# Performance work log

Hardware: AMD Instinct MI355X
Metric: run time of the kernel (lower is better)

Reference implementation:

```python
import jax, jax.numpy as jnp
import numpy as np

B, S, D = 32, 512, 512      # batch, seq_len, d_model
H, K = 16, 32               # head_num, head_dim
A = 256                     # attention_hidden_dim


def setup_inputs() -> dict:
    key = jax.random.key(0)
    ks = jax.random.split(key, 10)
    s = lambda fan_in: 1.0 / np.sqrt(fan_in)
    return {
        "x":   jax.random.normal(ks[0], (B, S, D), dtype=jnp.float32),
        # per-head Q projections: Linear(D, D), stored [H, in, out]
        "Qw":  jax.random.normal(ks[1], (H, D, D), dtype=jnp.float32) * s(D),
        "Qb":  jax.random.normal(ks[2], (H, D), dtype=jnp.float32) * s(D),
        # per-head V projections: Linear(D, K)
        "Vw":  jax.random.normal(ks[3], (H, D, K), dtype=jnp.float32) * s(D),
        "Vb":  jax.random.normal(ks[4], (H, K), dtype=jnp.float32) * s(D),
        # additive attention pooling: Linear(H*K, A) then Linear(A, 1)
        "Wv":  jax.random.normal(ks[5], (H * K, A), dtype=jnp.float32) * s(H * K),
        "bv":  jax.random.normal(ks[6], (A,), dtype=jnp.float32) * s(H * K),
        "wq":  jax.random.normal(ks[7], (A, 1), dtype=jnp.float32) * s(A),
        "bq":  jax.random.normal(ks[8], (1,), dtype=jnp.float32) * s(A),
    }


def reference(x, Qw, Qb, Vw, Vb, Wv, bv, wq, bq):
    # per-head query projection: [B, H, S, D]
    q = jnp.einsum("bsd,hde->bhse", x, Qw) + Qb[None, :, None, :]
    # raw scores: [B, H, S, S] (s = query pos, t = key pos)
    scores = jnp.einsum("bhse,bte->bhst", q, x)
    # NOTE: softmax over dim=-2 (the QUERY axis), not the usual key axis
    attn = jax.nn.softmax(scores, axis=-2)
    # context: [B, H, S, D]
    ctx = jnp.einsum("bhst,btd->bhsd", attn, x)
    # per-head value projection then concat heads -> [B, S, H*K]
    head_out = jnp.einsum("bhsd,hdk->bshk", ctx, Vw) + Vb[None, None, :, :]
    h = head_out.reshape(B, S, H * K)
    # dropout is identity at inference
    # additive attention pooling
    a = jnp.tanh(h @ Wv + bv) @ wq + bq          # [B, S, 1]
    z = jnp.einsum("bs,bsk->bk", a[..., 0], h)   # [B, H*K]
    return z
```

## Files before the change

kernel.cpp:

```cpp
#include <hip/hip_runtime.h>

#define DEVFN __device__ __forceinline__

typedef _Float16 f16;
typedef _Float16 f16x8 __attribute__((ext_vector_type(8)));
typedef _Float16 f16x4 __attribute__((ext_vector_type(4)));
typedef _Float16 f16x2 __attribute__((ext_vector_type(2)));
typedef float    f32x4 __attribute__((ext_vector_type(4)));

enum { NB = 32, NS = 512, ND = 512, NH = 16, NK = 32, NA = 256 };

#define SZ(x) ((size_t)(x))

typedef __attribute__((address_space(3))) void       as3_void;
typedef const __attribute__((address_space(1))) void as1_cvoid;
DEVFN void ldsdma16(const void* g, void* l) {
  __builtin_amdgcn_global_load_lds((as1_cvoid*)g, (as3_void*)l, 16, 0, 0);
}

DEVFN int xcd_swz(int flat, int n) {
  return (flat & 7) * (n >> 3) + (flat >> 3);
}

DEVFN void gemm256_pipe(const f16* __restrict__ Ag, const f16* __restrict__ Bg,
                        int lda, int ldb, f16* smem, f32x4 acc[8][4]) {
  const int tid  = threadIdx.x;
  const int lane = tid & 63;
  const int wid  = tid >> 6;
  const int wr   = wid >> 2;
  const int wcn  = wid & 3;
  const int s_r    = tid >> 2;
  const int s_gsrc = (tid & 3) ^ (s_r & 3);
  const int frow = lane & 15;
  const int fg   = lane >> 4;

  auto stage = [&](int t) {
    f16* buf = smem + (t & 3) * 16384;
    const f16* As = Ag + t * 32;
    const f16* Bs = Bg + t * 32;
#pragma unroll
    for (int j = 0; j < 2; ++j)
      ldsdma16(As + SZ(j * 128 + s_r) * lda + s_gsrc * 8, buf + j * 4096 + tid * 8);
#pragma unroll
    for (int j = 0; j < 2; ++j)
      ldsdma16(Bs + SZ(j * 128 + s_r) * ldb + s_gsrc * 8, buf + 8192 + j * 4096 + tid * 8);
  };

  stage(0); stage(1); stage(2);

  for (int t = 0; t < 16; ++t) {
    if (t <= 13)      asm volatile("s_waitcnt vmcnt(8)" ::: "memory");
    else if (t == 14) asm volatile("s_waitcnt vmcnt(4)" ::: "memory");
    else              asm volatile("s_waitcnt vmcnt(0)" ::: "memory");
    __builtin_amdgcn_s_barrier();
    if (t < 13) stage(t + 3);

    const f16* bufA = smem + (t & 3) * 16384;
    const f16* bufB = bufA + 8192;
    f16x8 af[8], bf[4];
#pragma unroll
    for (int mi = 0; mi < 8; ++mi) {
      int r_ = wr * 128 + mi * 16 + frow;
      af[mi] = *(const f16x8*)(bufA + r_ * 32 + ((fg ^ (r_ & 3)) * 8));
    }
#pragma unroll
    for (int ni = 0; ni < 4; ++ni) {
      int r_ = wcn * 64 + ni * 16 + frow;
      bf[ni] = *(const f16x8*)(bufB + r_ * 32 + ((fg ^ (r_ & 3)) * 8));
    }
    __builtin_amdgcn_s_setprio(1);
#pragma unroll
    for (int mi = 0; mi < 8; ++mi)
#pragma unroll
      for (int ni = 0; ni < 4; ++ni)
        acc[mi][ni] = __builtin_amdgcn_mfma_f32_16x16x32_f16(af[mi], bf[ni], acc[mi][ni], 0, 0, 0);
    __builtin_amdgcn_s_setprio(0);
  }
}

DEVFN void gemm_core_128(const f16* __restrict__ Ag, const f16* __restrict__ Bg,
                         int lda, int ldb, int nk, f16* lds, f32x4 acc[4][4]) {
  f16* As = lds;
  f16* Bs = lds + 128 * 64;
  const int tid  = threadIdx.x;
  const int lane = tid & 63;
  const int wvid = tid >> 6, wr = wvid >> 1, wc = wvid & 1;
  const int srow = tid >> 3, scol = (tid & 7) * 8;
  const int frow = lane & 15, fk = (lane >> 4) * 8;
  for (int ks = 0; ks < nk; ++ks) {
    const f16* ga = Ag + ks * 64 + scol;
    const f16* gb = Bg + ks * 64 + scol;
#pragma unroll
    for (int r = 0; r < 4; ++r) {
      ldsdma16(ga + SZ(r * 32 + srow) * lda, As + SZ(r * 32 + srow) * 64 + scol);
      ldsdma16(gb + SZ(r * 32 + srow) * ldb, Bs + SZ(r * 32 + srow) * 64 + scol);
    }
    __syncthreads();
#pragma unroll
    for (int kk = 0; kk < 64; kk += 32) {
      f16x8 a[4], b[4];
#pragma unroll
      for (int i = 0; i < 4; ++i)
        a[i] = *(const f16x8*)(As + SZ(wr * 64 + i * 16 + frow) * 64 + kk + fk);
#pragma unroll
      for (int j = 0; j < 4; ++j)
        b[j] = *(const f16x8*)(Bs + SZ(wc * 64 + j * 16 + frow) * 64 + kk + fk);
#pragma unroll
      for (int i = 0; i < 4; ++i)
#pragma unroll
        for (int j = 0; j < 4; ++j)
          acc[i][j] = __builtin_amdgcn_mfma_f32_16x16x32_f16(a[i], b[j], acc[i][j], 0, 0, 0);
    }
    __syncthreads();
  }
}

DEVFN void wlds_write(f16* wlds, int row, int col, f16 v) {
  int byte = (row * 256 + col * 2) ^ ((row & 7) << 4);
  *(f16*)((char*)wlds + byte) = v;
}
DEVFN f16x8 wlds_read8(const f16* wlds, int row, int col) {
  int byte = (row * 256 + col * 2) ^ ((row & 7) << 4);
  return *(const f16x8*)((const char*)wlds + byte);
}

__global__ __launch_bounds__(256) void k_cast4(const float* __restrict__ s,
                                               f16* __restrict__ d, int n4) {
  int i = blockIdx.x * 256 + threadIdx.x;
  if (i >= n4) return;
  float4 v = ((const float4*)s)[i];
  f16x4 o; o[0] = (f16)v.x; o[1] = (f16)v.y; o[2] = (f16)v.z; o[3] = (f16)v.w;
  ((f16x4*)d)[i] = o;
}

__global__ void k_tcast(const float* __restrict__ src, f16* __restrict__ dst,
                        int R, int C, long sStride, long dStride) {
  __shared__ float tile[32][33];
  src += (long)blockIdx.z * sStride;
  dst += (long)blockIdx.z * dStride;
  int c0 = blockIdx.x * 32, r0 = blockIdx.y * 32;
  int tx = threadIdx.x, ty = threadIdx.y;
#pragma unroll
  for (int i = 0; i < 4; ++i)
    tile[ty + 8 * i][tx] = src[(long)(r0 + ty + 8 * i) * C + c0 + tx];
  __syncthreads();
#pragma unroll
  for (int i = 0; i < 4; ++i)
    dst[(long)(c0 + ty + 8 * i) * R + r0 + tx] = (f16)tile[tx][ty + 8 * i];
}

__global__ __launch_bounds__(256) void k_gemm_xv(const f16* __restrict__ xh,
                                                 const f16* __restrict__ vwt,
                                                 f16* __restrict__ xvt) {
  __shared__ f16 smem[128 * 64 * 2];
  int z = blockIdx.z, b = z >> 2, hg = z & 3, tm = blockIdx.x;
  f32x4 acc[4][4] = {};
  gemm_core_128(xh + SZ(b) * NS * ND + SZ(tm) * 128 * ND,
                vwt + SZ(hg) * 4 * NK * ND, ND, ND, ND / 64, smem, acc);
  int tid = threadIdx.x, lane = tid & 63, wvid = tid >> 6, wr = wvid >> 1, wc = wvid & 1;
  int rbase = (lane >> 4) * 4, cbase = lane & 15;
#pragma unroll
  for (int mi = 0; mi < 4; ++mi)
#pragma unroll
    for (int ni = 0; ni < 4; ++ni) {
      int n = wc * 64 + ni * 16 + cbase;
      int hh = hg * 4 + (n >> 5), kk = n & 31;
#pragma unroll
      for (int r = 0; r < 4; ++r) {
        int t = tm * 128 + wr * 64 + mi * 16 + rbase + r;
        xvt[(SZ(b * NH + hh) * NK + kk) * NS + t] = (f16)acc[mi][ni][r];
      }
    }
}

__global__ __launch_bounds__(512, 2) void k_gemm_q256(const f16* __restrict__ xh,
                                                      const f16* __restrict__ qwt,
                                                      const float* __restrict__ Qb,
                                                      f16* __restrict__ qc, int b0) {
  __shared__ f16 smem[65536];
  int n = gridDim.x;
  int lg = xcd_swz(blockIdx.x, n);
  int tm2 = lg & 1, tn2 = (lg >> 1) & 1, bhl = lg >> 2;
  int b = b0 + (bhl >> 4), h = bhl & 15;
  f32x4 acc[8][4] = {};
  gemm256_pipe(xh + SZ(b) * NS * ND + SZ(tm2) * 256 * ND,
               qwt + SZ(h) * ND * ND + SZ(tn2) * 256 * ND, ND, ND, smem, acc);
  int lane = threadIdx.x & 63, wid = threadIdx.x >> 6;
  int wr = wid >> 2, wcn = wid & 3;
  int rbase = (lane >> 4) * 4, cbase = lane & 15;
  f16* qb = qc + SZ(bhl) * NS * ND;
#pragma unroll
  for (int mi = 0; mi < 8; ++mi)
#pragma unroll
    for (int ni = 0; ni < 4; ++ni) {
      int colg = tn2 * 256 + wcn * 64 + ni * 16 + cbase;
      float bias = Qb[h * ND + colg];
#pragma unroll
      for (int r = 0; r < 4; ++r) {
        int rowg = tm2 * 256 + wr * 128 + mi * 16 + rbase + r;
        qb[SZ(rowg) * ND + colg] = (f16)(acc[mi][ni][r] + bias);
      }
    }
}

__global__ __launch_bounds__(512, 2) void k_scores256(const f16* __restrict__ qc,
                                                      const f16* __restrict__ xh,
                                                      f16* __restrict__ sc,
                                                      float* __restrict__ mp,
                                                      float* __restrict__ zp, int b0) {
  __shared__ f16 smem[65536];
  int n = gridDim.x;
  int lg = xcd_swz(blockIdx.x, n);
  int st2 = lg & 1, tt2 = (lg >> 1) & 1, bhl = lg >> 2;
  int b = b0 + (bhl >> 4);
  f32x4 acc[8][4] = {};
  gemm256_pipe(qc + SZ(bhl) * NS * ND + SZ(st2) * 256 * ND,
               xh + SZ(b) * NS * ND + SZ(tt2) * 256 * ND, ND, ND, smem, acc);
  int tid = threadIdx.x, lane = tid & 63, wid = tid >> 6;
  int wr = wid >> 2, wcn = wid & 3;
  __syncthreads();
  float* sbuf = (float*)smem;

  float mh[4];
#pragma unroll
  for (int ni = 0; ni < 4; ++ni) {
    float m = -1e30f;
#pragma unroll
    for (int mi = 0; mi < 8; ++mi)
#pragma unroll
      for (int r = 0; r < 4; ++r) m = fmaxf(m, acc[mi][ni][r]);
    m = fmaxf(m, __shfl_xor(m, 16));
    m = fmaxf(m, __shfl_xor(m, 32));
    mh[ni] = m;
  }
  if (lane < 16) {
#pragma unroll
    for (int ni = 0; ni < 4; ++ni)
      sbuf[wr * 256 + wcn * 64 + ni * 16 + lane] = mh[ni];
  }
  __syncthreads();
  int cb_ = lane & 15;
  float tmc[4];
#pragma unroll
  for (int ni = 0; ni < 4; ++ni) {
    int col = wcn * 64 + ni * 16 + cb_;
    tmc[ni] = fmaxf(sbuf[col], sbuf[256 + col]);
  }
  f16x4* scb = (f16x4*)(sc + SZ(lg) * 65536);
  float sm[4] = {0.f, 0.f, 0.f, 0.f};
#pragma unroll
  for (int mi = 0; mi < 8; ++mi)
#pragma unroll
    for (int ni = 0; ni < 4; ++ni) {
      f16x4 o;
#pragma unroll
      for (int r = 0; r < 4; ++r) {
        float ev = __expf(acc[mi][ni][r] - tmc[ni]);
        o[r] = (f16)ev;
        sm[ni] += ev;
      }
      scb[((wid * 8 + mi) * 4 + ni) * 64 + lane] = o;
    }
#pragma unroll
  for (int ni = 0; ni < 4; ++ni) {
    sm[ni] += __shfl_xor(sm[ni], 16);
    sm[ni] += __shfl_xor(sm[ni], 32);
  }
  if (lane < 16) {
#pragma unroll
    for (int ni = 0; ni < 4; ++ni)
      sbuf[512 + wr * 256 + wcn * 64 + ni * 16 + lane] = sm[ni];
  }
  __syncthreads();
  if (tid < 256) {
    float m  = fmaxf(sbuf[tid], sbuf[256 + tid]);
    float zz = sbuf[512 + tid] + sbuf[768 + tid];
    size_t idx = (SZ(bhl) * 2 + st2) * NS + tt2 * 256 + tid;
    mp[idx] = m; zp[idx] = zz;
  }
}

__global__ __launch_bounds__(256) void k_stats_combine(const float* __restrict__ mp,
                                                       const float* __restrict__ zp,
                                                       float* __restrict__ cs) {
  int i = blockIdx.x * 256 + threadIdx.x;
  int bhl = i >> 9, t = i & (NS - 1);
  float m0 = mp[(SZ(bhl) * 2 + 0) * NS + t];
  float m1 = mp[(SZ(bhl) * 2 + 1) * NS + t];
  float m = fmaxf(m0, m1);
  float e0 = __expf(m0 - m), e1 = __expf(m1 - m);
  float Z = zp[(SZ(bhl) * 2 + 0) * NS + t] * e0 + zp[(SZ(bhl) * 2 + 1) * NS + t] * e1;
  float rZ = 1.0f / Z;
  cs[(SZ(bhl) * 2 + 0) * NS + t] = e0 * rZ;
  cs[(SZ(bhl) * 2 + 1) * NS + t] = e1 * rZ;
}

__global__ __launch_bounds__(256) void k_norm_pv(const f16* __restrict__ sc,
                                                 const f16* __restrict__ xvt,
                                                 const float* __restrict__ cs,
                                                 const float* __restrict__ Vb,
                                                 f16* __restrict__ h16, int b0) {
  __shared__ f16 wlds[128 * 128];
  int bhl = blockIdx.y, b = b0 + (bhl >> 4), h = bhl & 15;
  int st = blockIdx.x;
  int tid = threadIdx.x, lane = tid & 63, wvid = tid >> 6, wr = wvid >> 1, wc = wvid & 1;
  int rbase = (lane >> 4) * 4, cbase = lane & 15, fk = (lane >> 4) * 8;
  f32x4 acc2[2][2] = {};
  const f16* xvh = xvt + SZ(b * NH + h) * NK * NS;
  for (int tt = 0; tt < 4; ++tt) {
    int blk = (bhl * 2 + (tt >> 1)) * 2 + (st >> 1);
    const f16x4* scb = (const f16x4*)(sc + SZ(blk) * 65536);
    int wave_sc = (st & 1) * 4 + ((tt & 1) * 2 + wc);
#pragma unroll
    for (int ni = 0; ni < 4; ++ni) {
      int tl = wc * 64 + ni * 16 + cbase;
      float csv = cs[(SZ(bhl) * 2 + (st >> 1)) * NS + tt * 128 + tl];
#pragma unroll
      for (int mi = 0; mi < 4; ++mi) {
        int mi_sc = wr * 4 + mi;
        f16x4 v = scb[((wave_sc * 8 + mi_sc) * 4 + ni) * 64 + lane];
#pragma unroll
        for (int r = 0; r < 4; ++r) {
          int sl = wr * 64 + mi * 16 + rbase + r;
          wlds_write(wlds, sl, tl, (f16)((float)v[r] * csv));
        }
      }
    }
    __syncthreads();
    const f16* xvb = xvh + tt * 128;
#pragma unroll
    for (int tc = 0; tc < 4; ++tc) {
      f16x8 aw[2], bx[2];
#pragma unroll
      for (int m2 = 0; m2 < 2; ++m2)
        aw[m2] = wlds_read8(wlds, wvid * 32 + m2 * 16 + cbase, tc * 32 + fk);
#pragma unroll
      for (int n2 = 0; n2 < 2; ++n2)
        bx[n2] = *(const f16x8*)(xvb + SZ(n2 * 16 + cbase) * NS + tc * 32 + fk);
#pragma unroll
      for (int m2 = 0; m2 < 2; ++m2)
#pragma unroll
        for (int n2 = 0; n2 < 2; ++n2)
          acc2[m2][n2] = __builtin_amdgcn_mfma_f32_16x16x32_f16(aw[m2], bx[n2], acc2[m2][n2], 0, 0, 0);
    }
    __syncthreads();
  }
  const float* vb = Vb + h * NK;
#pragma unroll
  for (int m2 = 0; m2 < 2; ++m2)
#pragma unroll
    for (int n2 = 0; n2 < 2; ++n2)
#pragma unroll
      for (int r = 0; r < 4; ++r) {
        int sg = st * 128 + wvid * 32 + m2 * 16 + rbase + r;
        int kk = n2 * 16 + cbase;
        float val = acc2[m2][n2][r] + vb[kk];
        h16[SZ(b * NS + sg) * (NH * NK) + h * NK + kk] = (f16)val;
      }
}

__global__ __launch_bounds__(256) void k_gemm_u(const f16* __restrict__ h16,
                                                const f16* __restrict__ wvt,
                                                const float* __restrict__ bv,
                                                f16* __restrict__ U) {
  __shared__ f16 smem[128 * 64 * 2];
  int tm = blockIdx.x, tn = blockIdx.y;
  f32x4 acc[4][4] = {};
  gemm_core_128(h16 + SZ(tm) * 128 * ND, wvt + SZ(tn) * 128 * ND, ND, ND, ND / 64, smem, acc);
  int tid = threadIdx.x, lane = tid & 63, wvid = tid >> 6, wr = wvid >> 1, wc = wvid & 1;
  int rbase = (lane >> 4) * 4, cbase = lane & 15;
#pragma unroll
  for (int mi = 0; mi < 4; ++mi)
#pragma unroll
    for (int ni = 0; ni < 4; ++ni) {
      int colg = tn * 128 + wc * 64 + ni * 16 + cbase;
      float bias = bv[colg];
#pragma unroll
      for (int r = 0; r < 4; ++r) {
        int rowg = tm * 128 + wr * 64 + mi * 16 + rbase + r;
        U[SZ(rowg) * NA + colg] = (f16)tanhf(acc[mi][ni][r] + bias);
      }
    }
}

__global__ __launch_bounds__(256) void k_a(const f16* __restrict__ U,
                                           const float* __restrict__ wq,
                                           const float* __restrict__ bq,
                                           float* __restrict__ a) {
  int wid = (blockIdx.x * 256 + threadIdx.x) >> 6;
  int lane = threadIdx.x & 63;
  const f16* u = U + SZ(wid) * NA;
  float p = 0.f;
#pragma unroll
  for (int j = 0; j < NA / 64; ++j) p += (float)u[lane + 64 * j] * wq[lane + 64 * j];
#pragma unroll
  for (int o = 32; o; o >>= 1) p += __shfl_xor(p, o);
  if (lane == 0) a[wid] = p + bq[0];
}

__global__ __launch_bounds__(256) void k_zpart(const f16* __restrict__ h16,
                                               const float* __restrict__ a,
                                               float* __restrict__ zpt) {
  int b = blockIdx.y, c = blockIdx.x, tid = threadIdx.x;
  float z0 = 0.f, z1 = 0.f;
  for (int s = 0; s < 64; ++s) {
    int sg = c * 64 + s;
    float av = a[b * NS + sg];
    const f16* hr = h16 + SZ(b * NS + sg) * (NH * NK);
    f16x2 v = ((const f16x2*)hr)[tid];
    z0 += av * (float)v[0];
    z1 += av * (float)v[1];
  }
  zpt[SZ(b * 8 + c) * 512 + 2 * tid]     = z0;
  zpt[SZ(b * 8 + c) * 512 + 2 * tid + 1] = z1;
}

__global__ __launch_bounds__(256) void k_zred(const float* __restrict__ zpt,
                                              float* __restrict__ out) {
  int i = blockIdx.x * 256 + threadIdx.x;
  int b = i >> 9, k = i & 511;
  float z = 0.f;
#pragma unroll
  for (int c = 0; c < 8; ++c) z += zpt[SZ(b * 8 + c) * 512 + k];
  out[i] = z;
}

static size_t ws_plan(int cb, size_t off[14]) {
  size_t o = 0;
  auto put = [&](size_t bytes) { size_t r = o; o += (bytes + 255) & ~SZ(255); return r; };
  off[0]  = put(SZ(NB) * NS * ND * 2);
  off[1]  = put(SZ(NH) * ND * ND * 2);
  off[2]  = put(SZ(NA) * ND * 2);
  off[3]  = put(SZ(NH) * NK * ND * 2);
  off[4]  = put(SZ(NB) * NH * NK * NS * 2);
  off[5]  = put(SZ(cb) * NH * NS * ND * 2);
  off[6]  = put(SZ(cb) * NH * NS * NS * 2);
  off[7]  = put(SZ(cb) * NH * 2 * NS * 4);
  off[8]  = put(SZ(cb) * NH * 2 * NS * 4);
  off[9]  = put(SZ(cb) * NH * 2 * NS * 4);
  off[10] = put(SZ(NB) * NS * NH * NK * 2);
  off[11] = put(SZ(NB) * NS * NA * 2);
  off[12] = put(SZ(NB) * NS * 4);
  off[13] = put(SZ(NB) * 8 * NH * NK * 4);
  return o;
}

extern "C" void kernel_launch(void* const* d_in, const int* in_sizes, int n_in,
                              void* d_out, int out_size, void* d_ws, size_t ws_size,
                              hipStream_t stream) {
  const float* x  = (const float*)d_in[0];
  const float* Qw = (const float*)d_in[1];
  const float* Qb = (const float*)d_in[2];
  const float* Vw = (const float*)d_in[3];
  const float* Vb = (const float*)d_in[4];
  const float* Wv = (const float*)d_in[5];
  const float* bv = (const float*)d_in[6];
  const float* wq = (const float*)d_in[7];
  const float* bq = (const float*)d_in[8];

  int cbv = 0;
  size_t off[14];
  const int cand[5] = {32, 16, 8, 4, 2};
  for (int ci = 0; ci < 5; ++ci) {
    if (ws_plan(cand[ci], off) <= ws_size) { cbv = cand[ci]; break; }
  }
  if (cbv == 0) return;

  char* ws = (char*)d_ws;
  f16*   xh   = (f16*)(ws + off[0]);
  f16*   qwt  = (f16*)(ws + off[1]);
  f16*   wvt  = (f16*)(ws + off[2]);
  f16*   vwt  = (f16*)(ws + off[3]);
  f16*   xvt  = (f16*)(ws + off[4]);
  f16*   qc   = (f16*)(ws + off[5]);
  f16*   sc   = (f16*)(ws + off[6]);
  float* mp   = (float*)(ws + off[7]);
  float* zps  = (float*)(ws + off[8]);
  float* cs   = (float*)(ws + off[9]);
  f16*   h16  = (f16*)(ws + off[10]);
  f16*   U    = (f16*)(ws + off[11]);
  float* a    = (float*)(ws + off[12]);
  float* zpt  = (float*)(ws + off[13]);
  float* zout = (float*)d_out;

  k_cast4<<<SZ(NB) * NS * ND / 4 / 256, 256, 0, stream>>>(x, xh, NB * NS * ND / 4);
  k_tcast<<<dim3(16, 16, 16), dim3(32, 8), 0, stream>>>(Qw, qwt, ND, ND, (long)ND * ND, (long)ND * ND);
  k_tcast<<<dim3(8, 16, 1), dim3(32, 8), 0, stream>>>(Wv, wvt, ND, NA, 0, 0);
  k_tcast<<<dim3(1, 16, 16), dim3(32, 8), 0, stream>>>(Vw, vwt, ND, NK, (long)ND * NK, (long)NK * ND);
  k_gemm_xv<<<dim3(4, 1, NB * 4), 256, 0, stream>>>(xh, vwt, xvt);

  for (int b0 = 0; b0 < NB; b0 += cbv) {
    k_gemm_q256<<<cbv * 64, 512, 0, stream>>>(xh, qwt, Qb, qc, b0);
    k_scores256<<<cbv * 64, 512, 0, stream>>>(qc, xh, sc, mp, zps, b0);
    k_stats_combine<<<cbv * NH * NS / 256, 256, 0, stream>>>(mp, zps, cs);
    k_norm_pv<<<dim3(4, cbv * NH), 256, 0, stream>>>(sc, xvt, cs, Vb, h16, b0);
  }

  k_gemm_u<<<dim3(NB * NS / 128, 2, 1), 256, 0, stream>>>(h16, wvt, bv, U);
  k_a<<<NB * NS / 4, 256, 0, stream>>>(U, wq, bq, a);
  k_zpart<<<dim3(8, NB), 256, 0, stream>>>(h16, a, zpt);
  k_zred<<<NB * 512 / 256, 256, 0, stream>>>(zpt, zout);
}
```

Baseline: 548.2 us.

## Split 256-tile GEMM loop into two half-phases interleaving LDS DMA with MFMA

Restructures the main K-loop of the 256x256 GEMM so each k-step runs two half-tile phases of MFMA. The A-tile and B-tile DMA issues are spread across the phases, and explicit barriers plus sched_barriers fence the LDS reads from the matrix ops. The goal is better overlap of global-to-LDS loads and LDS fragment reads with MFMA work, and lower register pressure, since only 4 A fragments are live at once. The cost is four workgroup barriers per iteration instead of one, which adds synchronization overhead.

```diff
diff --git a/kernel.cpp b/kernel.cpp
--- a/kernel.cpp
+++ b/kernel.cpp
@@ -34,47 +34,72 @@
   const int frow = lane & 15;
   const int fg   = lane >> 4;
 
-  auto stage = [&](int t) {
+  auto stageA = [&](int t) {
     f16* buf = smem + (t & 3) * 16384;
     const f16* As = Ag + t * 32;
+    ldsdma16(As + SZ(s_r) * lda + s_gsrc * 8,       buf + tid * 8);
+    ldsdma16(As + SZ(128 + s_r) * lda + s_gsrc * 8, buf + 4096 + tid * 8);
+  };
+  auto stageB = [&](int t) {
+    f16* buf = smem + (t & 3) * 16384 + 8192;
     const f16* Bs = Bg + t * 32;
-#pragma unroll
-    for (int j = 0; j < 2; ++j)
-      ldsdma16(As + SZ(j * 128 + s_r) * lda + s_gsrc * 8, buf + j * 4096 + tid * 8);
-#pragma unroll
-    for (int j = 0; j < 2; ++j)
-      ldsdma16(Bs + SZ(j * 128 + s_r) * ldb + s_gsrc * 8, buf + 8192 + j * 4096 + tid * 8);
+    ldsdma16(Bs + SZ(s_r) * ldb + s_gsrc * 8,       buf + tid * 8);
+    ldsdma16(Bs + SZ(128 + s_r) * ldb + s_gsrc * 8, buf + 4096 + tid * 8);
   };
-
-  stage(0); stage(1); stage(2);
+  auto rdA = [&](const f16* bufA, int mi) -> f16x8 {
+    int r_ = wr * 128 + mi * 16 + frow;
+    return *(const f16x8*)(bufA + r_ * 32 + ((fg ^ (r_ & 3)) * 8));
+  };
+  auto rdB = [&](const f16* bufB, int ni) -> f16x8 {
+    int r_ = wcn * 64 + ni * 16 + frow;
+    return *(const f16x8*)(bufB + r_ * 32 + ((fg ^ (r_ & 3)) * 8));
+  };
+
+  stageA(0); stageB(0); stageA(1); stageB(1); stageA(2); stageB(2);
+  asm volatile("s_waitcnt vmcnt(8)" ::: "memory");
+  __builtin_amdgcn_s_barrier();
 
   for (int t = 0; t < 16; ++t) {
-    if (t <= 13)      asm volatile("s_waitcnt vmcnt(8)" ::: "memory");
-    else if (t == 14) asm volatile("s_waitcnt vmcnt(4)" ::: "memory");
-    else              asm volatile("s_waitcnt vmcnt(0)" ::: "memory");
-    __builtin_amdgcn_s_barrier();
-    if (t < 13) stage(t + 3);
-
     const f16* bufA = smem + (t & 3) * 16384;
     const f16* bufB = bufA + 8192;
-    f16x8 af[8], bf[4];
-#pragma unroll
-    for (int mi = 0; mi < 8; ++mi) {
-      int r_ = wr * 128 + mi * 16 + frow;
-      af[mi] = *(const f16x8*)(bufA + r_ * 32 + ((fg ^ (r_ & 3)) * 8));
-    }
-#pragma unroll
-    for (int ni = 0; ni < 4; ++ni) {
-      int r_ = wcn * 64 + ni * 16 + frow;
-      bf[ni] = *(const f16x8*)(bufB + r_ * 32 + ((fg ^ (r_ & 3)) * 8));
-    }
+    f16x8 af[4], bf[4];
+
+#pragma unroll
+    for (int mi = 0; mi < 4; ++mi) af[mi] = rdA(bufA, mi);
+#pragma unroll
+    for (int ni = 0; ni < 4; ++ni) bf[ni] = rdB(bufB, ni);
+    if (t < 13) stageA(t + 3);
+    __builtin_amdgcn_s_barrier();
+    asm volatile("s_waitcnt lgkmcnt(0)" ::: "memory");
+    __builtin_amdgcn_sched_barrier(0);
     __builtin_amdgcn_s_setprio(1);
 #pragma unroll
-    for (int mi = 0; mi < 8; ++mi)
+    for (int mi = 0; mi < 4; ++mi)
 #pragma unroll
       for (int ni = 0; ni < 4; ++ni)
         acc[mi][ni] = __builtin_amdgcn_mfma_f32_16x16x32_f16(af[mi], bf[ni], acc[mi][ni], 0, 0, 0);
     __builtin_amdgcn_s_setprio(0);
+    __builtin_amdgcn_sched_barrier(0);
+    __builtin_amdgcn_s_barrier();
+
+#pragma unroll
+    for (int mi = 0; mi < 4; ++mi) af[mi] = rdA(bufA, 4 + mi);
+    if (t < 13) stageB(t + 3);
+    if (t <= 12)      asm volatile("s_waitcnt vmcnt(8)" ::: "memory");
+    else if (t == 13) asm volatile("s_waitcnt vmcnt(4)" ::: "memory");
+    else              asm volatile("s_waitcnt vmcnt(0)" ::: "memory");
+    __builtin_amdgcn_s_barrier();
+    asm volatile("s_waitcnt lgkmcnt(0)" ::: "memory");
+    __builtin_amdgcn_sched_barrier(0);
+    __builtin_amdgcn_s_setprio(1);
+#pragma unroll
+    for (int mi = 0; mi < 4; ++mi)
+#pragma unroll
+      for (int ni = 0; ni < 4; ++ni)
+        acc[4 + mi][ni] = __builtin_amdgcn_mfma_f32_16x16x32_f16(af[mi], bf[ni], acc[4 + mi][ni], 0, 0, 0);
+    __builtin_amdgcn_s_setprio(0);
+    __builtin_amdgcn_sched_barrier(0);
+    __builtin_amdgcn_s_barrier();
   }
 }
 
```

Result: slower. 561.6 us (+2.4%).

## Restructure 256-tile GEMM into 4-phase ping-pong pipeline with BK=64

Applied to the files above, without the earlier changes.

Rewrites the 256x256 GEMM main loop to use K-steps of 64 with double-buffered LDS instead of K-steps of 32 with quad buffering. Each iteration is split into four quadrant phases, with LDS-DMA staging of half-tiles interleaved between phases and separated by barriers and sched_barriers. An 8-wide XOR swizzle replaces the 4-wide one. The goal is to overlap global-to-LDS transfers and LDS reads with MFMA work and to halve loop iterations. In exchange it adds more barriers and tight vmcnt bookkeeping, which risks stalls or subtle hazards.

```diff
diff --git a/kernel.cpp b/kernel.cpp
--- a/kernel.cpp
+++ b/kernel.cpp
@@ -29,53 +29,105 @@
   const int wid  = tid >> 6;
   const int wr   = wid >> 2;
   const int wcn  = wid & 3;
-  const int s_r    = tid >> 2;
-  const int s_gsrc = (tid & 3) ^ (s_r & 3);
+  const int s_r  = tid >> 3;
+  const int s_g  = tid & 7;
   const int frow = lane & 15;
   const int fg   = lane >> 4;
 
-  auto stage = [&](int t) {
-    f16* buf = smem + (t & 3) * 16384;
-    const f16* As = Ag + t * 32;
-    const f16* Bs = Bg + t * 32;
-#pragma unroll
-    for (int j = 0; j < 2; ++j)
-      ldsdma16(As + SZ(j * 128 + s_r) * lda + s_gsrc * 8, buf + j * 4096 + tid * 8);
-#pragma unroll
-    for (int j = 0; j < 2; ++j)
-      ldsdma16(Bs + SZ(j * 128 + s_r) * ldb + s_gsrc * 8, buf + 8192 + j * 4096 + tid * 8);
+  auto stageA = [&](int t, int h) {
+    f16* base = smem + (t & 1) * 32768;
+    const f16* G = Ag + t * 64;
+#pragma unroll
+    for (int j = 0; j < 2; ++j) {
+      int row = j * 128 + h * 64 + s_r;
+      ldsdma16(G + SZ(row) * lda + ((s_g ^ (row & 7)) * 8), base + row * 64 + s_g * 8);
+    }
   };
-
-  stage(0); stage(1); stage(2);
-
-  for (int t = 0; t < 16; ++t) {
-    if (t <= 13)      asm volatile("s_waitcnt vmcnt(8)" ::: "memory");
-    else if (t == 14) asm volatile("s_waitcnt vmcnt(4)" ::: "memory");
-    else              asm volatile("s_waitcnt vmcnt(0)" ::: "memory");
+  auto stageB = [&](int t, int h) {
+    f16* base = smem + (t & 1) * 32768 + 16384;
+    const f16* G = Bg + t * 64;
+#pragma unroll
+    for (int j = 0; j < 2; ++j) {
+      int row = (j * 2 + (s_r >> 5)) * 64 + h * 32 + (s_r & 31);
+      ldsdma16(G + SZ(row) * ldb + ((s_g ^ (row & 7)) * 8), base + row * 64 + s_g * 8);
+    }
+  };
+  auto rdA = [&](int t, int row, int kk) -> f16x8 {
+    const f16* base = smem + (t & 1) * 32768;
+    return *(const f16x8*)(base + row * 64 + (((kk * 4 + fg) ^ (row & 7)) * 8));
+  };
+  auto rdB = [&](int t, int row, int kk) -> f16x8 {
+    const f16* base = smem + (t & 1) * 32768 + 16384;
+    return *(const f16x8*)(base + row * 64 + (((kk * 4 + fg) ^ (row & 7)) * 8));
+  };
+
+  f16x8 af[8], bf0[4], bf1[4];
+
+#define QUAD(a, b, BF)                                                          \
+  _Pragma("unroll")                                                             \
+  for (int mi = 0; mi < 4; ++mi)                                                \
+    _Pragma("unroll")                                                           \
+    for (int ni = 0; ni < 2; ++ni)                                              \
+      _Pragma("unroll")                                                         \
+      for (int kk = 0; kk < 2; ++kk)                                            \
+        acc[(a)*4 + mi][(b)*2 + ni] = __builtin_amdgcn_mfma_f32_16x16x32_f16(   \
+            af[mi * 2 + kk], BF[ni * 2 + kk], acc[(a)*4 + mi][(b)*2 + ni], 0, 0, 0);
+
+#define PHASE_TAIL(MFMA_BLOCK)                              \
+  __builtin_amdgcn_s_barrier();                             \
+  asm volatile("s_waitcnt lgkmcnt(0)" ::: "memory");        \
+  __builtin_amdgcn_sched_barrier(0);                        \
+  __builtin_amdgcn_s_setprio(1);                            \
+  MFMA_BLOCK                                                \
+  __builtin_amdgcn_s_setprio(0);                            \
+  __builtin_amdgcn_sched_barrier(0);
+
+  stageA(0, 0); stageB(0, 0); stageB(0, 1); stageA(0, 1);
+  stageA(1, 0); stageB(1, 0); stageB(1, 1);
+  asm volatile("s_waitcnt vmcnt(6)" ::: "memory");
+  __builtin_amdgcn_s_barrier();
+
+  for (int t = 0; t < 8; ++t) {
+#pragma unroll
+    for (int mi = 0; mi < 4; ++mi)
+#pragma unroll
+      for (int kk = 0; kk < 2; ++kk)
+        af[mi * 2 + kk] = rdA(t, wr * 128 + mi * 16 + frow, kk);
+#pragma unroll
+    for (int ni = 0; ni < 2; ++ni)
+#pragma unroll
+      for (int kk = 0; kk < 2; ++kk)
+        bf0[ni * 2 + kk] = rdB(t, wcn * 64 + ni * 16 + frow, kk);
+    if (t <= 6) stageA(t + 1, 1);
+    PHASE_TAIL(QUAD(0, 0, bf0))
     __builtin_amdgcn_s_barrier();
-    if (t < 13) stage(t + 3);
-
-    const f16* bufA = smem + (t & 3) * 16384;
-    const f16* bufB = bufA + 8192;
-    f16x8 af[8], bf[4];
-#pragma unroll
-    for (int mi = 0; mi < 8; ++mi) {
-      int r_ = wr * 128 + mi * 16 + frow;
-      af[mi] = *(const f16x8*)(bufA + r_ * 32 + ((fg ^ (r_ & 3)) * 8));
-    }
-#pragma unroll
-    for (int ni = 0; ni < 4; ++ni) {
-      int r_ = wcn * 64 + ni * 16 + frow;
-      bf[ni] = *(const f16x8*)(bufB + r_ * 32 + ((fg ^ (r_ & 3)) * 8));
-    }
-    __builtin_amdgcn_s_setprio(1);
-#pragma unroll
-    for (int mi = 0; mi < 8; ++mi)
-#pragma unroll
-      for (int ni = 0; ni < 4; ++ni)
-        acc[mi][ni] = __builtin_amdgcn_mfma_f32_16x16x32_f16(af[mi], bf[ni], acc[mi][ni], 0, 0, 0);
-    __builtin_amdgcn_s_setprio(0);
-  }
+
+#pragma unroll
+    for (int ni = 0; ni < 2; ++ni)
+#pragma unroll
+      for (int kk = 0; kk < 2; ++kk)
+        bf1[ni * 2 + kk] = rdB(t, wcn * 64 + 32 + ni * 16 + frow, kk);
+    if (t <= 5) stageA(t + 2, 0);
+    PHASE_TAIL(QUAD(0, 1, bf1))
+    __builtin_amdgcn_s_barrier();
+
+#pragma unroll
+    for (int mi = 0; mi < 4; ++mi)
+#pragma unroll
+      for (int kk = 0; kk < 2; ++kk)
+        af[mi * 2 + kk] = rdA(t, wr * 128 + 64 + mi * 16 + frow, kk);
+    if (t <= 5) stageB(t + 2, 0);
+    PHASE_TAIL(QUAD(1, 1, bf1))
+    __builtin_amdgcn_s_barrier();
+
+    if (t <= 5) stageB(t + 2, 1);
+    PHASE_TAIL(QUAD(1, 0, bf0))
+    if (t < 6)       asm volatile("s_waitcnt vmcnt(6)" ::: "memory");
+    else if (t == 6) asm volatile("s_waitcnt vmcnt(0)" ::: "memory");
+    __builtin_amdgcn_s_barrier();
+  }
+#undef QUAD
+#undef PHASE_TAIL
 }
 
 DEVFN void gemm_core_128(const f16* __restrict__ Ag, const f16* __restrict__ Bg,
```

After: 509.2 us. 1.08x faster.
